# Performance work log

Hardware: AMD Instinct MI355X
Metric: run time of the kernel (lower is better)

## Reference

```python
import jax, jax.numpy as jnp
import numpy as np

B, C, H, W, E, HEADS = 8, 128, 96, 96, 16, 4
HD = C // HEADS

def _ln(x, g, b, eps=1e-5):
    m = jnp.mean(x, axis=-1, keepdims=True)
    v = jnp.mean(jnp.square(x - m), axis=-1, keepdims=True)
    return (x - m) * jax.lax.rsqrt(v + eps) * g + b

def _gelu(x):
    return jax.nn.gelu(x, approximate=False)  # torch nn.GELU default (erf)

def setup_inputs() -> dict:
    key = jax.random.key(0)
    ks = iter(jax.random.split(key, 48))
    def wgt(shape, s=0.02):
        return jax.random.normal(next(ks), shape, jnp.float32) * s
    d = {
        "feature_map": jax.random.normal(next(ks), (B, C, H, W), jnp.float32),
        "hyperedge_scores": jax.random.uniform(next(ks), (B, H * W, E), jnp.float32),
        # norm_node_pre
        "np_g": jnp.ones((C,), jnp.float32), "np_b": jnp.zeros((C,), jnp.float32),
        # MultiheadAttention (self-attn over hyperedges)
        "mha_w_in": wgt((3 * C, C)), "mha_b_in": jnp.zeros((3 * C,), jnp.float32),
        "mha_w_out": wgt((C, C)), "mha_b_out": jnp.zeros((C,), jnp.float32),
        # transformer FFN
        "ffn_w1": wgt((2 * C, C)), "ffn_b1": jnp.zeros((2 * C,), jnp.float32),
        "ffn_w2": wgt((C, 2 * C)), "ffn_b2": jnp.zeros((C,), jnp.float32),
        # shared LayerNorm inside HypergraphTransformerConv (used twice)
        "tnorm_g": jnp.ones((C,), jnp.float32), "tnorm_b": jnp.zeros((C,), jnp.float32),
        # norm_hyper
        "nh_g": jnp.ones((C,), jnp.float32), "nh_b": jnp.zeros((C,), jnp.float32),
        # hyper_proj
        "hp_w": wgt((C, C)), "hp_b": jnp.zeros((C,), jnp.float32),
        # HyperedgeGuidedNodeAttention
        "q_w": wgt((C, C)), "q_b": jnp.zeros((C,), jnp.float32),
        "kv_w": wgt((2 * C, C)), "kv_b": jnp.zeros((2 * C,), jnp.float32),
        # norm_fusion
        "nf_g": jnp.ones((2 * C,), jnp.float32), "nf_b": jnp.zeros((2 * C,), jnp.float32),
        # gate = Linear(2C->C) + LayerNorm(C) + Sigmoid
        "gate_w": wgt((C, 2 * C)), "gate_b": jnp.zeros((C,), jnp.float32),
        "gate_ln_g": jnp.ones((C,), jnp.float32), "gate_ln_b": jnp.zeros((C,), jnp.float32),
        # node_proj
        "nproj_w": wgt((C, C)), "nproj_b": jnp.zeros((C,), jnp.float32),
    }
    return d

def _forward(feature_map, hyperedge_scores, np_g, np_b, mha_w_in, mha_b_in,
             mha_w_out, mha_b_out, ffn_w1, ffn_b1, ffn_w2, ffn_b2,
             tnorm_g, tnorm_b, nh_g, nh_b, hp_w, hp_b, q_w, q_b, kv_w, kv_b,
             nf_g, nf_b, gate_w, gate_b, gate_ln_g, gate_ln_b, nproj_w, nproj_b):
    b, c, h, w = feature_map.shape
    n = h * w
    node = jnp.transpose(feature_map.reshape(b, c, n), (0, 2, 1))   # [B,N,C]
    node = _ln(node, np_g, np_b)
    # hyperedge aggregation: H^T @ X -> [B,E,C]
    hyper = jnp.einsum('bne,bnc->bec', hyperedge_scores, node)
    # --- HypergraphTransformerConv (self-attn over E=16 hyperedges) ---
    qkv = hyper @ mha_w_in.T + mha_b_in                               # [B,E,3C]
    q, k, v = jnp.split(qkv, 3, axis=-1)
    def heads(x):  # [B,E,C] -> [B,h,E,hd]
        return jnp.transpose(x.reshape(b, E, HEADS, HD), (0, 2, 1, 3))
    q, k, v = heads(q), heads(k), heads(v)
    attn = jax.nn.softmax(jnp.einsum('bhqd,bhkd->bhqk', q, k) / np.sqrt(HD), axis=-1)
    ao = jnp.einsum('bhqk,bhkd->bhqd', attn, v)
    ao = jnp.transpose(ao, (0, 2, 1, 3)).reshape(b, E, c)
    ao = ao @ mha_w_out.T + mha_b_out
    x = _ln(hyper + ao, tnorm_g, tnorm_b)
    ffn = _gelu(x @ ffn_w1.T + ffn_b1) @ ffn_w2.T + ffn_b2
    hyper = _ln(x + ffn, tnorm_g, tnorm_b)
    # ---
    hyper = _ln(hyper, nh_g, nh_b)
    hyper = _gelu(hyper @ hp_w.T + hp_b)                              # [B,E,C]
    intra = jnp.einsum('bne,bec->bnc', hyperedge_scores, hyper)       # [B,N,C]
    # HyperedgeGuidedNodeAttention (scale = C**-0.5)
    Q = node @ q_w.T + q_b
    K, V = jnp.split(hyper @ kv_w.T + kv_b, 2, axis=-1)
    a = jax.nn.softmax(jnp.einsum('bnc,bec->bne', Q, K) * (c ** -0.5), axis=-1)
    cross = jnp.einsum('bne,bec->bnc', a, V)
    combined = _ln(jnp.concatenate([intra, cross], axis=-1), nf_g, nf_b)
    gate = jax.nn.sigmoid(_ln(combined @ gate_w.T + gate_b, gate_ln_g, gate_ln_b))
    fused = gate * intra + (1.0 - gate) * cross
    upd = node + fused                                                # dropout in eval mode
    out = _gelu(upd @ nproj_w.T + nproj_b)
    return jnp.transpose(out, (0, 2, 1)).reshape(b, c, h, w)

def reference(feature_map, hyperedge_scores, np_g, np_b, mha_w_in, mha_b_in,
              mha_w_out, mha_b_out, ffn_w1, ffn_b1, ffn_w2, ffn_b2,
              tnorm_g, tnorm_b, nh_g, nh_b, hp_w, hp_b, q_w, q_b, kv_w, kv_b,
              nf_g, nf_b, gate_w, gate_b, gate_ln_g, gate_ln_b, nproj_w, nproj_b):
    return _forward(feature_map, hyperedge_scores, np_g, np_b, mha_w_in, mha_b_in,
                    mha_w_out, mha_b_out, ffn_w1, ffn_b1, ffn_w2, ffn_b2,
                    tnorm_g, tnorm_b, nh_g, nh_b, hp_w, hp_b, q_w, q_b, kv_w, kv_b,
                    nf_g, nf_b, gate_w, gate_b, gate_ln_g, gate_ln_b, nproj_w, nproj_b)
```

## Files before the change

### kernel.cpp

```cpp
#include <hip/hip_runtime.h>

typedef unsigned short bf_t;
typedef unsigned int u32;
typedef short short8 __attribute__((ext_vector_type(8)));
typedef float f32x4 __attribute__((ext_vector_type(4)));

#define NB 8
#define CC 128
#define NN 9216
#define EE 16
#define NT 144

__device__ __forceinline__ float b2f(bf_t u){ return __uint_as_float(((u32)u)<<16); }
__device__ __forceinline__ bf_t f2b(float f){
  u32 u = __float_as_uint(f);
  u = (u + 0x7fffu + ((u>>16)&1u)) >> 16;
  return (bf_t)u;
}
__device__ __forceinline__ float gelu_f(float x){ return 0.5f*x*(1.f+erff(x*0.70710678118654752f)); }
__device__ __forceinline__ float red16(float v){
  #pragma unroll
  for (int m=1;m<16;m<<=1) v += __shfl_xor(v, m, 16);
  return v;
}
__device__ __forceinline__ float grs(float var){
  return rsqrtf(fmaxf(var + 1e-5f, 1e-8f));
}
__device__ __forceinline__ short8 ldw8(const float* __restrict__ p){
  float4 a = *(const float4*)p;
  float4 b = *(const float4*)(p+4);
  short8 o;
  o[0]=(short)f2b(a.x); o[1]=(short)f2b(a.y); o[2]=(short)f2b(a.z); o[3]=(short)f2b(a.w);
  o[4]=(short)f2b(b.x); o[5]=(short)f2b(b.y); o[6]=(short)f2b(b.z); o[7]=(short)f2b(b.w);
  return o;
}

template<int MODE>
__global__ __launch_bounds__(256) void k_pre(float* __restrict__ hacc,
    const float* __restrict__ gw, const float* __restrict__ npw,
    bf_t* __restrict__ gwb, bf_t* __restrict__ npwb,
    const float* __restrict__ w_in, const float* __restrict__ w_out,
    const float* __restrict__ w1, const float* __restrict__ w2,
    const float* __restrict__ hpw, const float* __restrict__ kvw,
    const float* __restrict__ qw,
    bf_t* __restrict__ w_in_b, bf_t* __restrict__ w_out_b,
    bf_t* __restrict__ w1_b, bf_t* __restrict__ w2_b,
    bf_t* __restrict__ hpw_b, bf_t* __restrict__ kvw_b,
    bf_t* __restrict__ qwT_b){
  int i = blockIdx.x*256 + threadIdx.x;
  hacc[i] = 0.f;
  if (MODE >= 1){
    gwb[i]       = f2b(gw[i]);
    gwb[i+16384] = f2b(gw[i+16384]);
    npwb[i]      = f2b(npw[i]);
  }
  if (MODE == 2){
    #pragma unroll
    for (int k=0;k<3;k++) w_in_b[i + k*16384] = f2b(w_in[i + k*16384]);
    w_out_b[i]       = f2b(w_out[i]);
    w1_b[i]          = f2b(w1[i]);
    w1_b[i+16384]    = f2b(w1[i+16384]);
    w2_b[i]          = f2b(w2[i]);
    w2_b[i+16384]    = f2b(w2[i+16384]);
    hpw_b[i]         = f2b(hpw[i]);
    kvw_b[i]         = f2b(kvw[i]);
    kvw_b[i+16384]   = f2b(kvw[i+16384]);
    qwT_b[i]         = f2b(qw[(i&127)*128 + (i>>7)]);
  }
}

template<int BFOUT, int ATOM>
__global__ __launch_bounds__(256,4) void k_ln_agg(const float* __restrict__ fm,
                                                  const float* __restrict__ g,
                                                  const float* __restrict__ bb,
                                                  const float* __restrict__ sc,
                                                  float* __restrict__ nln,
                                                  bf_t* __restrict__ nlnb,
                                                  float* __restrict__ hacc,
                                                  float* __restrict__ part){
  int b = blockIdx.y, n0 = blockIdx.x*64, tid = threadIdx.x;
  __shared__ float xs[128*65];
  __shared__ float scs[64][17];
  __shared__ float ps[4][64], pq[4][64], mrs[2][64];
  const float* base = fm + (size_t)b*CC*NN + n0;
  #pragma unroll
  for (int p=0;p<8;p++){
    int idx = tid + p*256;
    int c = idx>>4, n4 = (idx&15)*4;
    float4 v = *(const float4*)(base + (size_t)c*NN + n4);
    xs[c*65 + n4+0] = v.x; xs[c*65 + n4+1] = v.y;
    xs[c*65 + n4+2] = v.z; xs[c*65 + n4+3] = v.w;
  }
  { int n = tid>>2, e4 = (tid&3)*4;
    float4 sv = *(const float4*)(sc + ((size_t)(b*NN + n0 + n))*EE + e4);
    scs[n][e4+0] = sv.x; scs[n][e4+1] = sv.y;
    scs[n][e4+2] = sv.z; scs[n][e4+3] = sv.w;
  }
  __syncthreads();
  { int cg = tid>>6, n = tid&63;
    float s=0.f, q=0.f;
    #pragma unroll
    for (int c=0;c<32;c++){ float v = xs[(cg*32+c)*65 + n]; s+=v; q+=v*v; }
    ps[cg][n]=s; pq[cg][n]=q;
  }
  __syncthreads();
  if (tid < 64){
    float S = ps[0][tid]+ps[1][tid]+ps[2][tid]+ps[3][tid];
    float Q = pq[0][tid]+pq[1][tid]+pq[2][tid]+pq[3][tid];
    float m = S*(1.f/128.f);
    mrs[0][tid] = m; mrs[1][tid] = grs(Q*(1.f/128.f) - m*m);
  }
  __syncthreads();
  #pragma unroll
  for (int p=0;p<8;p++){
    int idx = tid + p*256;
    int c = idx>>4, n4 = (idx&15)*4;
    float gv = g[c], bv = bb[c];
    float v0 = (xs[c*65+n4+0]-mrs[0][n4+0])*mrs[1][n4+0]*gv + bv;
    float v1 = (xs[c*65+n4+1]-mrs[0][n4+1])*mrs[1][n4+1]*gv + bv;
    float v2 = (xs[c*65+n4+2]-mrs[0][n4+2])*mrs[1][n4+2]*gv + bv;
    float v3 = (xs[c*65+n4+3]-mrs[0][n4+3])*mrs[1][n4+3]*gv + bv;
    xs[c*65+n4+0]=v0; xs[c*65+n4+1]=v1; xs[c*65+n4+2]=v2; xs[c*65+n4+3]=v3;
    if (!BFOUT){
      float4 o; o.x=v0; o.y=v1; o.z=v2; o.w=v3;
      *(float4*)(nln + ((size_t)(b*CC + c))*NN + n0 + n4) = o;
    }
  }
  __syncthreads();
  if (BFOUT){
    #pragma unroll
    for (int p=0;p<4;p++){
      int idx = tid + p*256;
      int n = idx>>4, c8 = (idx&15)*8;
      short8 o;
      #pragma unroll
      for (int j=0;j<8;j++) o[j] = (short)f2b(xs[(c8+j)*65 + n]);
      *(short8*)(nlnb + ((size_t)(b*NN + n0 + n))*CC + c8) = o;
    }
  }
  { int cp = tid&63, eh = tid>>6;
    float a0[4]={0,0,0,0}, a1[4]={0,0,0,0};
    for (int n=0;n<64;n++){
      float x0 = xs[cp*65 + n], x1 = xs[(cp+64)*65 + n];
      #pragma unroll
      for (int j=0;j<4;j++){
        float se = scs[n][eh*4+j];
        a0[j] += se*x0; a1[j] += se*x1;
      }
    }
    if (ATOM){
      #pragma unroll
      for (int j=0;j<4;j++){
        float* hb = hacc + (size_t)(b*EE + eh*4 + j)*CC;
        atomicAdd(hb + cp, a0[j]);
        atomicAdd(hb + cp + 64, a1[j]);
      }
    } else {
      float* pb = part + ((size_t)(b*NT + blockIdx.x)*EE)*CC;
      #pragma unroll
      for (int j=0;j<4;j++){
        pb[(eh*4+j)*CC + cp]      = a0[j];
        pb[(eh*4+j)*CC + cp + 64] = a1[j];
      }
    }
  }
}

__global__ __launch_bounds__(128) void k_red(const float* __restrict__ part,
                                             float* __restrict__ hacc){
  int e = blockIdx.x, b = blockIdx.y, c = threadIdx.x;
  const float* p = part + ((size_t)(b*NT)*EE + e)*CC + c;
  float s0=0.f, s1=0.f, s2=0.f, s3=0.f;
  #pragma unroll
  for (int t=0;t<NT;t+=4){
    s0 += p[(size_t)(t+0)*EE*CC];
    s1 += p[(size_t)(t+1)*EE*CC];
    s2 += p[(size_t)(t+2)*EE*CC];
    s3 += p[(size_t)(t+3)*EE*CC];
  }
  hacc[((size_t)b*EE + e)*CC + c] = (s0+s1)+(s2+s3);
}

template<int K, int NOUT, int ACT, int WB, int NW>
__device__ __forceinline__ void gemm16(const bf_t* A, int SA,
                                       const float* __restrict__ W,
                                       const bf_t* __restrict__ Wb,
                                       const float* __restrict__ bias,
                                       bf_t* O, int SO, int tid){
  int lane = tid&63, wid = tid>>6;
  int m16 = lane&15, quad = lane>>4;
  #pragma unroll
  for (int u=0; u<NOUT/(16*NW); u++){
    int n0 = u*(16*NW) + wid*16;
    f32x4 acc = {0.f,0.f,0.f,0.f};
    #pragma unroll
    for (int k0=0;k0<K;k0+=32){
      short8 af = *(const short8*)(A + m16*SA + k0 + quad*8);
      short8 bfv = WB ? *(const short8*)(Wb + (size_t)(n0+m16)*K + k0 + quad*8)
                      : ldw8(W + (size_t)(n0+m16)*K + k0 + quad*8);
      acc = __builtin_amdgcn_mfma_f32_16x16x32_bf16(af, bfv, acc, 0, 0, 0);
    }
    int col = n0 + m16;
    float bv = bias[col];
    #pragma unroll
    for (int r=0;r<4;r++){
      float v = acc[r] + bv;
      if (ACT) v = gelu_f(v);
      O[(quad*4+r)*SO + col] = f2b(v);
    }
  }
}

#define SP1 136
#define SP2 264
#define SP3 392

template<int WB>
__global__ __launch_bounds__(512) void k_edge(const float* __restrict__ hacc,
    const float* w_in, const float* b_in, const float* w_out, const float* b_out,
    const float* w1, const float* b1, const float* w2, const float* b2v,
    const float* tg, const float* tb, const float* nhg, const float* nhb,
    const float* hpw, const float* hpb, const float* kvw, const float* kvbias,
    const float* qw, const float* qb,
    const bf_t* __restrict__ w_in_b, const bf_t* __restrict__ w_out_b,
    const bf_t* __restrict__ w1_b, const bf_t* __restrict__ w2_b,
    const bf_t* __restrict__ hpw_b, const bf_t* __restrict__ kvw_b,
    const bf_t* __restrict__ qwT_b,
    bf_t* __restrict__ hfw, bf_t* __restrict__ vws,
    bf_t* __restrict__ Ktgb, float* __restrict__ qbK){
  __shared__ __align__(16) bf_t hyp0[16*SP1];
  __shared__ __align__(16) bf_t qkvb[16*SP3];
  __shared__ __align__(16) bf_t aob [16*SP1];
  __shared__ __align__(16) bf_t xnb [16*SP1];
  __shared__ __align__(16) bf_t h1b [16*SP2];
  __shared__ __align__(16) bf_t t2b [16*SP1];
  __shared__ __align__(16) bf_t hfb [16*SP1];
  __shared__ __align__(16) bf_t kvo [16*SP2];
  int b = blockIdx.x, tid = threadIdx.x;
  int lane = tid&63, wid = tid>>6, m16 = lane&15, quad = lane>>4;

  #pragma unroll
  for (int p=0;p<4;p++){
    int idx = tid + p*512;
    int e = idx>>7, c = idx&127;
    hyp0[e*SP1 + c] = f2b(hacc[(size_t)(b*EE + e)*CC + c]);
  }
  __syncthreads();
  gemm16<128,384,0,WB,8>(hyp0, SP1, w_in, w_in_b, b_in, qkvb, SP3, tid);
  __syncthreads();
  if (tid < 256){
    int part = tid&3, hq = tid>>2;
    int h = hq>>4, qi = hq&15;
    int dbase = h*32 + part*8;
    float qv[8];
    #pragma unroll
    for (int j=0;j<8;j++) qv[j] = b2f(qkvb[qi*SP3 + dbase + j]);
    float dot[16];
    #pragma unroll
    for (int kk=0;kk<16;kk++){
      float s = 0.f;
      #pragma unroll
      for (int j=0;j<8;j++) s += qv[j]*b2f(qkvb[kk*SP3 + 128 + dbase + j]);
      dot[kk] = s;
    }
    #pragma unroll
    for (int m=1;m<4;m<<=1){
      #pragma unroll
      for (int kk=0;kk<16;kk++) dot[kk] += __shfl_xor(dot[kk], m, 4);
    }
    const float sc1 = 0.17677669529663687f;
    float mx = -1e30f;
    #pragma unroll
    for (int kk=0;kk<16;kk++){ dot[kk] *= sc1; mx = fmaxf(mx, dot[kk]); }
    float sum = 0.f;
    #pragma unroll
    for (int kk=0;kk<16;kk++){ dot[kk] = __expf(dot[kk]-mx); sum += dot[kk]; }
    float inv = 1.f/sum;
    float ao[8] = {0,0,0,0,0,0,0,0};
    #pragma unroll
    for (int kk=0;kk<16;kk++){
      float p = dot[kk]*inv;
      #pragma unroll
      for (int j=0;j<8;j++) ao[j] += p*b2f(qkvb[kk*SP3 + 256 + dbase + j]);
    }
    #pragma unroll
    for (int j=0;j<8;j++) aob[qi*SP1 + dbase + j] = f2b(ao[j]);
  }
  __syncthreads();
  gemm16<128,128,0,WB,8>(aob, SP1, w_out, w_out_b, b_out, xnb, SP1, tid);
  __syncthreads();
  if (tid < 256){
    int e = tid>>4, i = tid&15;
    float v[8]; float s=0.f, q=0.f;
    #pragma unroll
    for (int j=0;j<8;j++){
      int c = i*8+j;
      v[j] = b2f(hyp0[e*SP1+c]) + b2f(xnb[e*SP1+c]);
      s += v[j]; q += v[j]*v[j];
    }
    s = red16(s); q = red16(q);
    float m = s*(1.f/128.f);
    float rs = grs(q*(1.f/128.f) - m*m);
    #pragma unroll
    for (int j=0;j<8;j++){
      int c = i*8+j;
      xnb[e*SP1+c] = f2b((v[j]-m)*rs*tg[c] + tb[c]);
    }
  }
  __syncthreads();
  gemm16<128,256,1,WB,8>(xnb, SP1, w1, w1_b, b1, h1b, SP2, tid);
  __syncthreads();
  gemm16<256,128,0,WB,8>(h1b, SP2, w2, w2_b, b2v, aob, SP1, tid);
  __syncthreads();
  if (tid < 256){
    int e = tid>>4, i = tid&15;
    float v[8]; float s=0.f, q=0.f;
    #pragma unroll
    for (int j=0;j<8;j++){
      int c = i*8+j;
      v[j] = b2f(xnb[e*SP1+c]) + b2f(aob[e*SP1+c]);
      s += v[j]; q += v[j]*v[j];
    }
    s = red16(s); q = red16(q);
    float m = s*(1.f/128.f);
    float rs = grs(q*(1.f/128.f) - m*m);
    float s2=0.f, q2=0.f;
    #pragma unroll
    for (int j=0;j<8;j++){
      int c = i*8+j;
      v[j] = (v[j]-m)*rs*tg[c] + tb[c];
      s2 += v[j]; q2 += v[j]*v[j];
    }
    s2 = red16(s2); q2 = red16(q2);
    float m2 = s2*(1.f/128.f);
    float rs2 = grs(q2*(1.f/128.f) - m2*m2);
    #pragma unroll
    for (int j=0;j<8;j++){
      int c = i*8+j;
      t2b[e*SP1+c] = f2b((v[j]-m2)*rs2*nhg[c] + nhb[c]);
    }
  }
  __syncthreads();
  gemm16<128,128,1,WB,8>(t2b, SP1, hpw, hpw_b, hpb, hfb, SP1, tid);
  __syncthreads();
  gemm16<128,256,0,WB,8>(hfb, SP1, kvw, kvw_b, kvbias, kvo, SP2, tid);
  __syncthreads();
  #pragma unroll
  for (int p=0;p<4;p++){
    int idx = tid + p*512;
    int e = idx>>7, c = idx&127;
    size_t o = (size_t)(b*EE + e)*CC + c;
    hfw[o] = hfb[e*SP1 + c];
    vws[o] = kvo[e*SP2 + 128 + c];
  }
  {
    int n0 = wid*16;
    f32x4 acc = {0.f,0.f,0.f,0.f};
    #pragma unroll
    for (int k0=0;k0<128;k0+=32){
      short8 a = *(const short8*)(kvo + m16*SP2 + k0 + quad*8);
      short8 bq;
      if (WB){
        bq = *(const short8*)(qwT_b + (size_t)(n0+m16)*128 + k0 + quad*8);
      } else {
        #pragma unroll
        for (int j=0;j<8;j++)
          bq[j] = (short)f2b(qw[(size_t)(k0+quad*8+j)*128 + n0+m16]);
      }
      acc = __builtin_amdgcn_mfma_f32_16x16x32_bf16(a, bq, acc, 0, 0, 0);
    }
    #pragma unroll
    for (int r=0;r<4;r++)
      Ktgb[(size_t)(b*EE + quad*4 + r)*CC + n0 + m16] = f2b(acc[r]);
  }
  if (tid < 256){
    int e = tid>>4, i = tid&15;
    float s = 0.f;
    #pragma unroll
    for (int j=0;j<8;j++) s += qb[i*8+j]*b2f(kvo[e*SP2 + i*8+j]);
    s = red16(s);
    if (i == 0) qbK[b*EE + e] = s;
  }
}

template<int MODE>
__global__ __launch_bounds__(256,3) void k_meganode(
    float* __restrict__ io, const bf_t* __restrict__ nlnb,
    const float* __restrict__ sc,
    const bf_t* __restrict__ hf, const bf_t* __restrict__ vw,
    const bf_t* __restrict__ ktg, const float* __restrict__ qbK,
    const float* __restrict__ nfg, const float* __restrict__ nfb,
    const float* __restrict__ gw, const bf_t* __restrict__ gwb,
    const float* __restrict__ gb,
    const float* __restrict__ glng, const float* __restrict__ glnb,
    const float* __restrict__ npw, const bf_t* __restrict__ npwb,
    const float* __restrict__ npb){
  int tid = threadIdx.x, lane = tid&63, wid = tid>>6;
  int m16 = lane&15, quad = lane>>4;
  int b = blockIdx.y, n0 = blockIdx.x*64;
  __shared__ __align__(16) char sm[34816];
  bf_t* xt  = (bf_t*)(sm);
  bf_t* ktT = (bf_t*)(sm + 17408);
  bf_t* hfT = (bf_t*)(sm + 21760);
  bf_t* vfT = (bf_t*)(sm + 25856);
  bf_t* ash = (bf_t*)(sm + 29952);
  bf_t* ct  = (bf_t*)(sm + 17408);
  float* ot = (float*)(sm);
  const short8 z8 = {0,0,0,0,0,0,0,0};

  if (MODE == 2){
    const bf_t* nb = nlnb + ((size_t)(b*NN + n0))*CC;
    #pragma unroll
    for (int p=0;p<4;p++){
      int idx = tid + p*256;
      int n = idx>>4, c8 = (idx&15)*8;
      *(short8*)&xt[n*136 + c8] = *(const short8*)(nb + (size_t)n*CC + c8);
    }
  } else {
    #pragma unroll
    for (int p=0;p<8;p++){
      int idx = tid + p*256;
      int c = idx>>4, n4 = (idx&15)*4;
      float4 v = *(const float4*)(io + ((size_t)(b*CC + c))*NN + n0 + n4);
      xt[(n4+0)*136 + c] = f2b(v.x);
      xt[(n4+1)*136 + c] = f2b(v.y);
      xt[(n4+2)*136 + c] = f2b(v.z);
      xt[(n4+3)*136 + c] = f2b(v.w);
    }
  }
  { const u32* kp = (const u32*)(ktg + (size_t)b*EE*CC);
    #pragma unroll
    for (int p=0;p<4;p++){
      int idx = tid + p*256;
      int e = idx>>6, c2 = (idx&63)*2;
      *(u32*)&ktT[e*136 + c2] = kp[idx];
    }
  }
  { const u32* hs = (const u32*)(hf + (size_t)b*EE*CC);
    const u32* vs = (const u32*)(vw + (size_t)b*EE*CC);
    #pragma unroll
    for (int p=0;p<4;p++){
      int idx = tid + p*256;
      int e = idx>>6, c2 = (idx&63)*2;
      u32 hv = hs[idx], vv = vs[idx];
      hfT[(c2+0)*16 + e] = (bf_t)(hv&0xffffu);
      hfT[(c2+1)*16 + e] = (bf_t)(hv>>16);
      vfT[(c2+0)*16 + e] = (bf_t)(vv&0xffffu);
      vfT[(c2+1)*16 + e] = (bf_t)(vv>>16);
    }
  }
  __syncthreads();

  f32x4 dacc = {0.f,0.f,0.f,0.f};
  #pragma unroll
  for (int kk=0;kk<4;kk++){
    short8 a = *(const short8*)(xt + (wid*16+m16)*136 + kk*32 + quad*8);
    short8 bfr = *(const short8*)(ktT + m16*136 + kk*32 + quad*8);
    dacc = __builtin_amdgcn_mfma_f32_16x16x32_bf16(a, bfr, dacc, 0, 0, 0);
  }
  { float qbe = qbK[b*EE + m16];
    #pragma unroll
    for (int r=0;r<4;r++){
      float v = (dacc[r] + qbe) * 0.08838834764831845f;
      float m = v;
      #pragma unroll
      for (int msk=1;msk<16;msk<<=1) m = fmaxf(m, __shfl_xor(m, msk, 16));
      float ex = __expf(v - m);
      float s = ex;
      #pragma unroll
      for (int msk=1;msk<16;msk<<=1) s += __shfl_xor(s, msk, 16);
      ash[(wid*16 + quad*4 + r)*16 + m16] = f2b(ex / s);
    }
  }

  short8 scf = z8, asf = z8;
  if (quad < 2){
    const float* sp = sc + ((size_t)(b*NN + n0 + wid*16 + m16))*EE + quad*8;
    float4 u0 = *(const float4*)sp;
    float4 u1 = *(const float4*)(sp+4);
    scf[0]=(short)f2b(u0.x); scf[1]=(short)f2b(u0.y); scf[2]=(short)f2b(u0.z); scf[3]=(short)f2b(u0.w);
    scf[4]=(short)f2b(u1.x); scf[5]=(short)f2b(u1.y); scf[6]=(short)f2b(u1.z); scf[7]=(short)f2b(u1.w);
    asf = *(const short8*)(ash + (wid*16+m16)*16 + quad*8);
  }
  f32x4 acc_it[8], acc_cr[8];
  #pragma unroll
  for (int t=0;t<8;t++){
    short8 bh = z8, bv = z8;
    if (quad < 2){
      bh = *(const short8*)(hfT + (t*16+m16)*16 + quad*8);
      bv = *(const short8*)(vfT + (t*16+m16)*16 + quad*8);
    }
    f32x4 zf = {0.f,0.f,0.f,0.f};
    acc_it[t] = __builtin_amdgcn_mfma_f32_16x16x32_bf16(scf, bh, zf, 0, 0, 0);
    acc_cr[t] = __builtin_amdgcn_mfma_f32_16x16x32_bf16(asf, bv, zf, 0, 0, 0);
  }

  float mean4[4], rstd4[4];
  { float s4[4]={0,0,0,0}, q4[4]={0,0,0,0};
    #pragma unroll
    for (int t=0;t<8;t++)
      #pragma unroll
      for (int r=0;r<4;r++){
        float a = acc_it[t][r], c = acc_cr[t][r];
        s4[r] += a + c; q4[r] += a*a + c*c;
      }
    #pragma unroll
    for (int r=0;r<4;r++){
      s4[r] = red16(s4[r]); q4[r] = red16(q4[r]);
      mean4[r] = s4[r]*(1.f/256.f);
      rstd4[r] = grs(q4[r]*(1.f/256.f) - mean4[r]*mean4[r]);
    }
  }
  __syncthreads();
  short8 af[8];
  #pragma unroll
  for (int r=0;r<4;r++){
    int node = wid*16 + quad*4 + r;
    #pragma unroll
    for (int t=0;t<8;t++){
      int ch = t*16 + m16;
      ct[node*136 + ch] = f2b((acc_it[t][r]-mean4[r])*rstd4[r]*nfg[ch] + nfb[ch]);
    }
  }
  #pragma unroll
  for (int kk=0;kk<4;kk++)
    af[kk] = *(const short8*)(ct + (wid*16+m16)*136 + kk*32 + quad*8);
  #pragma unroll
  for (int r=0;r<4;r++){
    int node = wid*16 + quad*4 + r;
    #pragma unroll
    for (int t=0;t<8;t++){
      int ch = t*16 + m16;
      ct[node*136 + ch] = f2b((acc_cr[t][r]-mean4[r])*rstd4[r]*nfg[128+ch] + nfb[128+ch]);
    }
  }
  #pragma unroll
  for (int kk=0;kk<4;kk++)
    af[4+kk] = *(const short8*)(ct + (wid*16+m16)*136 + kk*32 + quad*8);

  f32x4 acc_g[8];
  #pragma unroll
  for (int t=0;t<8;t++){
    f32x4 a = {0.f,0.f,0.f,0.f};
    #pragma unroll
    for (int kk=0;kk<8;kk++){
      short8 w8 = (MODE >= 1) ? *(const short8*)(gwb + (size_t)(t*16+m16)*256 + kk*32 + quad*8)
                              : ldw8(gw + (size_t)(t*16+m16)*256 + kk*32 + quad*8);
      a = __builtin_amdgcn_mfma_f32_16x16x32_bf16(af[kk], w8, a, 0, 0, 0);
    }
    acc_g[t] = a;
  }

  { float s2[4]={0,0,0,0}, q2[4]={0,0,0,0};
    #pragma unroll
    for (int t=0;t<8;t++){
      float bv = gb[t*16+m16];
      #pragma unroll
      for (int r=0;r<4;r++){
        float v = acc_g[t][r] + bv;
        acc_g[t][r] = v; s2[r] += v; q2[r] += v*v;
      }
    }
    #pragma unroll
    for (int r=0;r<4;r++){ s2[r] = red16(s2[r]); q2[r] = red16(q2[r]); }
    #pragma unroll
    for (int t=0;t<8;t++){
      int col = t*16 + m16;
      float lg = glng[col], lb = glnb[col];
      #pragma unroll
      for (int r=0;r<4;r++){
        float m2 = s2[r]*(1.f/128.f);
        float rs2 = grs(q2[r]*(1.f/128.f) - m2*m2);
        float z = (acc_g[t][r]-m2)*rs2*lg + lb;
        float gs = 1.f/(1.f + __expf(-z));
        int node = wid*16 + quad*4 + r;
        float nld = b2f(xt[node*136 + col]);
        xt[node*136 + col] = f2b(nld + gs*acc_it[t][r] + (1.f-gs)*acc_cr[t][r]);
      }
    }
  }

  short8 bfu[4];
  #pragma unroll
  for (int kk=0;kk<4;kk++)
    bfu[kk] = *(const short8*)(xt + (wid*16+m16)*136 + kk*32 + quad*8);
  __syncthreads();
  #pragma unroll
  for (int mt=0;mt<8;mt++){
    f32x4 o = {0.f,0.f,0.f,0.f};
    #pragma unroll
    for (int kk=0;kk<4;kk++){
      short8 aw = (MODE >= 1) ? *(const short8*)(npwb + (size_t)(mt*16+m16)*128 + kk*32 + quad*8)
                              : ldw8(npw + (size_t)(mt*16+m16)*128 + kk*32 + quad*8);
      o = __builtin_amdgcn_mfma_f32_16x16x32_bf16(aw, bfu[kk], o, 0, 0, 0);
    }
    #pragma unroll
    for (int r=0;r<4;r++){
      int cp = mt*16 + quad*4 + r;
      ot[cp*68 + wid*16 + m16] = gelu_f(o[r] + npb[cp]);
    }
  }
  __syncthreads();
  #pragma unroll
  for (int p=0;p<8;p++){
    int idx = tid + p*256;
    int c = idx>>4, n4 = (idx&15)*4;
    float4 v = *(const float4*)&ot[c*68 + n4];
    *(float4*)(io + ((size_t)(b*CC + c))*NN + n0 + n4) = v;
  }
}

extern "C" void kernel_launch(void* const* d_in, const int* in_sizes, int n_in,
                              void* d_out, int out_size, void* d_ws, size_t ws_size,
                              hipStream_t stream){
  (void)in_sizes; (void)n_in; (void)out_size;
  const float* fm   = (const float*)d_in[0];
  const float* sc   = (const float*)d_in[1];
  const float* npg  = (const float*)d_in[2];
  const float* npb_ = (const float*)d_in[3];
  const float* w_in = (const float*)d_in[4];
  const float* b_in = (const float*)d_in[5];
  const float* w_out= (const float*)d_in[6];
  const float* b_out= (const float*)d_in[7];
  const float* w1   = (const float*)d_in[8];
  const float* b1   = (const float*)d_in[9];
  const float* w2   = (const float*)d_in[10];
  const float* b2v  = (const float*)d_in[11];
  const float* tg   = (const float*)d_in[12];
  const float* tb   = (const float*)d_in[13];
  const float* nhg  = (const float*)d_in[14];
  const float* nhb  = (const float*)d_in[15];
  const float* hpw  = (const float*)d_in[16];
  const float* hpb  = (const float*)d_in[17];
  const float* qw   = (const float*)d_in[18];
  const float* qb   = (const float*)d_in[19];
  const float* kvw  = (const float*)d_in[20];
  const float* kvb  = (const float*)d_in[21];
  const float* nfg  = (const float*)d_in[22];
  const float* nfb  = (const float*)d_in[23];
  const float* gw   = (const float*)d_in[24];
  const float* gb   = (const float*)d_in[25];
  const float* glng = (const float*)d_in[26];
  const float* glnb = (const float*)d_in[27];
  const float* npw  = (const float*)d_in[28];
  const float* npb2 = (const float*)d_in[29];

  float* nln = (float*)d_out;

  char* w = (char*)d_ws;
  float* hacc    = (float*)(w);
  float* qbK     = (float*)(w + 65536);
  bf_t*  hfw     = (bf_t*) (w + 66048);
  bf_t*  vws     = (bf_t*) (w + 98816);
  bf_t*  Ktgb    = (bf_t*) (w + 131584);
  bf_t*  gwb     = (bf_t*) (w + 164352);
  bf_t*  npwb    = (bf_t*) (w + 229888);
  bf_t*  w_in_b  = (bf_t*) (w + 262656);
  bf_t*  w_out_b = (bf_t*) (w + 360960);
  bf_t*  w1_b    = (bf_t*) (w + 393728);
  bf_t*  w2_b    = (bf_t*) (w + 459264);
  bf_t*  hpw_b   = (bf_t*) (w + 524800);
  bf_t*  kvw_b   = (bf_t*) (w + 557568);
  bf_t*  qwT_b   = (bf_t*) (w + 623104);
  bf_t*  nlnb    = (bf_t*) (w + 655872);
  float* part    = (float*)(w + 19530240);
  bool full2 = (ws_size >= (size_t)28967424);
  bool full  = (ws_size >= (size_t)19530240);
  bool pre   = (ws_size >= (size_t)262656);

  if (full2){
    k_pre<2><<<dim3(64), dim3(256), 0, stream>>>(hacc, gw, npw, gwb, npwb,
        w_in, w_out, w1, w2, hpw, kvw, qw,
        w_in_b, w_out_b, w1_b, w2_b, hpw_b, kvw_b, qwT_b);
    k_ln_agg<1,0><<<dim3(NT,8), dim3(256), 0, stream>>>(fm, npg, npb_, sc, nln, nlnb, hacc, part);
    k_red<<<dim3(EE,8), dim3(128), 0, stream>>>(part, hacc);
    k_edge<1><<<dim3(8), dim3(512), 0, stream>>>(hacc, w_in,b_in,w_out,b_out,
        w1,b1,w2,b2v, tg,tb, nhg,nhb, hpw,hpb, kvw,kvb, qw,qb,
        w_in_b, w_out_b, w1_b, w2_b, hpw_b, kvw_b, qwT_b,
        hfw, vws, Ktgb, qbK);
    k_meganode<2><<<dim3(NT,8), dim3(256), 0, stream>>>(nln, nlnb, sc, hfw, vws, Ktgb, qbK,
        nfg, nfb, gw, gwb, gb, glng, glnb, npw, npwb, npb2);
  } else if (full){
    k_pre<2><<<dim3(64), dim3(256), 0, stream>>>(hacc, gw, npw, gwb, npwb,
        w_in, w_out, w1, w2, hpw, kvw, qw,
        w_in_b, w_out_b, w1_b, w2_b, hpw_b, kvw_b, qwT_b);
    k_ln_agg<1,1><<<dim3(NT,8), dim3(256), 0, stream>>>(fm, npg, npb_, sc, nln, nlnb, hacc, part);
    k_edge<1><<<dim3(8), dim3(512), 0, stream>>>(hacc, w_in,b_in,w_out,b_out,
        w1,b1,w2,b2v, tg,tb, nhg,nhb, hpw,hpb, kvw,kvb, qw,qb,
        w_in_b, w_out_b, w1_b, w2_b, hpw_b, kvw_b, qwT_b,
        hfw, vws, Ktgb, qbK);
    k_meganode<2><<<dim3(NT,8), dim3(256), 0, stream>>>(nln, nlnb, sc, hfw, vws, Ktgb, qbK,
        nfg, nfb, gw, gwb, gb, glng, glnb, npw, npwb, npb2);
  } else if (pre){
    k_pre<1><<<dim3(64), dim3(256), 0, stream>>>(hacc, gw, npw, gwb, npwb,
        w_in, w_out, w1, w2, hpw, kvw, qw,
        w_in_b, w_out_b, w1_b, w2_b, hpw_b, kvw_b, qwT_b);
    k_ln_agg<0,1><<<dim3(NT,8), dim3(256), 0, stream>>>(fm, npg, npb_, sc, nln, nlnb, hacc, part);
    k_edge<0><<<dim3(8), dim3(512), 0, stream>>>(hacc, w_in,b_in,w_out,b_out,
        w1,b1,w2,b2v, tg,tb, nhg,nhb, hpw,hpb, kvw,kvb, qw,qb,
        w_in_b, w_out_b, w1_b, w2_b, hpw_b, kvw_b, qwT_b,
        hfw, vws, Ktgb, qbK);
    k_meganode<1><<<dim3(NT,8), dim3(256), 0, stream>>>(nln, nlnb, sc, hfw, vws, Ktgb, qbK,
        nfg, nfb, gw, gwb, gb, glng, glnb, npw, npwb, npb2);
  } else {
    k_pre<0><<<dim3(64), dim3(256), 0, stream>>>(hacc, gw, npw, gwb, npwb,
        w_in, w_out, w1, w2, hpw, kvw, qw,
        w_in_b, w_out_b, w1_b, w2_b, hpw_b, kvw_b, qwT_b);
    k_ln_agg<0,1><<<dim3(NT,8), dim3(256), 0, stream>>>(fm, npg, npb_, sc, nln, nlnb, hacc, part);
    k_edge<0><<<dim3(8), dim3(512), 0, stream>>>(hacc, w_in,b_in,w_out,b_out,
        w1,b1,w2,b2v, tg,tb, nhg,nhb, hpw,hpb, kvw,kvb, qw,qb,
        w_in_b, w_out_b, w1_b, w2_b, hpw_b, kvw_b, qwT_b,
        hfw, vws, Ktgb, qbK);
    k_meganode<0><<<dim3(NT,8), dim3(256), 0, stream>>>(nln, nlnb, sc, hfw, vws, Ktgb, qbK,
        nfg, nfb, gw, gwb, gb, glng, glnb, npw, npwb, npb2);
  }
}
```

Measured before the change: 267.5 us.

## Drop partial-sum reduction kernel, shrink meganode LDS and store output directly

Removes the partial-buffer plus separate reduction kernel path, so hyperedge aggregation always uses global atomics into hacc. In the node kernel, the fused-LayerNorm staging tile is narrowed to 72-wide halves, which cuts shared memory from 34816 to 32000 bytes. The LDS-transposed float4 output store is replaced with direct per-lane global writes, which drops two barriers. The intent is fewer launches and more occupancy, at the cost of atomic contention and less coalesced output stores (each store covers 16 contiguous floats per channel row).

```diff
diff --git a/kernel.cpp b/kernel.cpp
--- a/kernel.cpp
+++ b/kernel.cpp
@@ -69,15 +69,14 @@
   }
 }
 
-template<int BFOUT, int ATOM>
+template<int BFOUT>
 __global__ __launch_bounds__(256,4) void k_ln_agg(const float* __restrict__ fm,
                                                   const float* __restrict__ g,
                                                   const float* __restrict__ bb,
                                                   const float* __restrict__ sc,
                                                   float* __restrict__ nln,
                                                   bf_t* __restrict__ nlnb,
-                                                  float* __restrict__ hacc,
-                                                  float* __restrict__ part){
+                                                  float* __restrict__ hacc){
   int b = blockIdx.y, n0 = blockIdx.x*64, tid = threadIdx.x;
   __shared__ float xs[128*65];
   __shared__ float scs[64][17];
@@ -148,37 +147,13 @@
         a0[j] += se*x0; a1[j] += se*x1;
       }
     }
-    if (ATOM){
-      #pragma unroll
-      for (int j=0;j<4;j++){
-        float* hb = hacc + (size_t)(b*EE + eh*4 + j)*CC;
-        atomicAdd(hb + cp, a0[j]);
-        atomicAdd(hb + cp + 64, a1[j]);
-      }
-    } else {
-      float* pb = part + ((size_t)(b*NT + blockIdx.x)*EE)*CC;
-      #pragma unroll
-      for (int j=0;j<4;j++){
-        pb[(eh*4+j)*CC + cp]      = a0[j];
-        pb[(eh*4+j)*CC + cp + 64] = a1[j];
-      }
-    }
-  }
-}
-
-__global__ __launch_bounds__(128) void k_red(const float* __restrict__ part,
-                                             float* __restrict__ hacc){
-  int e = blockIdx.x, b = blockIdx.y, c = threadIdx.x;
-  const float* p = part + ((size_t)(b*NT)*EE + e)*CC + c;
-  float s0=0.f, s1=0.f, s2=0.f, s3=0.f;
-  #pragma unroll
-  for (int t=0;t<NT;t+=4){
-    s0 += p[(size_t)(t+0)*EE*CC];
-    s1 += p[(size_t)(t+1)*EE*CC];
-    s2 += p[(size_t)(t+2)*EE*CC];
-    s3 += p[(size_t)(t+3)*EE*CC];
-  }
-  hacc[((size_t)b*EE + e)*CC + c] = (s0+s1)+(s2+s3);
+    #pragma unroll
+    for (int j=0;j<4;j++){
+      float* hb = hacc + (size_t)(b*EE + eh*4 + j)*CC;
+      atomicAdd(hb + cp, a0[j]);
+      atomicAdd(hb + cp + 64, a1[j]);
+    }
+  }
 }
 
 template<int K, int NOUT, int ACT, int WB, int NW>
@@ -398,14 +373,13 @@
   int tid = threadIdx.x, lane = tid&63, wid = tid>>6;
   int m16 = lane&15, quad = lane>>4;
   int b = blockIdx.y, n0 = blockIdx.x*64;
-  __shared__ __align__(16) char sm[34816];
+  __shared__ __align__(16) char sm[32000];
   bf_t* xt  = (bf_t*)(sm);
   bf_t* ktT = (bf_t*)(sm + 17408);
   bf_t* hfT = (bf_t*)(sm + 21760);
   bf_t* vfT = (bf_t*)(sm + 25856);
   bf_t* ash = (bf_t*)(sm + 29952);
   bf_t* ct  = (bf_t*)(sm + 17408);
-  float* ot = (float*)(sm);
   const short8 z8 = {0,0,0,0,0,0,0,0};
 
   if (MODE == 2){
@@ -514,29 +488,35 @@
   __syncthreads();
   short8 af[8];
   #pragma unroll
-  for (int r=0;r<4;r++){
-    int node = wid*16 + quad*4 + r;
-    #pragma unroll
-    for (int t=0;t<8;t++){
-      int ch = t*16 + m16;
-      ct[node*136 + ch] = f2b((acc_it[t][r]-mean4[r])*rstd4[r]*nfg[ch] + nfb[ch]);
-    }
-  }
-  #pragma unroll
-  for (int kk=0;kk<4;kk++)
-    af[kk] = *(const short8*)(ct + (wid*16+m16)*136 + kk*32 + quad*8);
-  #pragma unroll
-  for (int r=0;r<4;r++){
-    int node = wid*16 + quad*4 + r;
-    #pragma unroll
-    for (int t=0;t<8;t++){
-      int ch = t*16 + m16;
-      ct[node*136 + ch] = f2b((acc_cr[t][r]-mean4[r])*rstd4[r]*nfg[128+ch] + nfb[128+ch]);
-    }
-  }
-  #pragma unroll
-  for (int kk=0;kk<4;kk++)
-    af[4+kk] = *(const short8*)(ct + (wid*16+m16)*136 + kk*32 + quad*8);
+  for (int s=0;s<2;s++){
+    #pragma unroll
+    for (int r=0;r<4;r++){
+      int node = wid*16 + quad*4 + r;
+      #pragma unroll
+      for (int t=0;t<4;t++){
+        int ch = (s*4+t)*16 + m16;
+        ct[node*72 + t*16 + m16] = f2b((acc_it[s*4+t][r]-mean4[r])*rstd4[r]*nfg[ch] + nfb[ch]);
+      }
+    }
+    #pragma unroll
+    for (int k2=0;k2<2;k2++)
+      af[s*2+k2] = *(const short8*)(ct + (wid*16+m16)*72 + k2*32 + quad*8);
+  }
+  #pragma unroll
+  for (int s=0;s<2;s++){
+    #pragma unroll
+    for (int r=0;r<4;r++){
+      int node = wid*16 + quad*4 + r;
+      #pragma unroll
+      for (int t=0;t<4;t++){
+        int ch = (s*4+t)*16 + m16;
+        ct[node*72 + t*16 + m16] = f2b((acc_cr[s*4+t][r]-mean4[r])*rstd4[r]*nfg[128+ch] + nfb[128+ch]);
+      }
+    }
+    #pragma unroll
+    for (int k2=0;k2<2;k2++)
+      af[4+s*2+k2] = *(const short8*)(ct + (wid*16+m16)*72 + k2*32 + quad*8);
+  }
 
   f32x4 acc_g[8];
   #pragma unroll
@@ -584,7 +564,6 @@
   #pragma unroll
   for (int kk=0;kk<4;kk++)
     bfu[kk] = *(const short8*)(xt + (wid*16+m16)*136 + kk*32 + quad*8);
-  __syncthreads();
   #pragma unroll
   for (int mt=0;mt<8;mt++){
     f32x4 o = {0.f,0.f,0.f,0.f};
@@ -597,16 +576,8 @@
     #pragma unroll
     for (int r=0;r<4;r++){
       int cp = mt*16 + quad*4 + r;
-      ot[cp*68 + wid*16 + m16] = gelu_f(o[r] + npb[cp]);
-    }
-  }
-  __syncthreads();
-  #pragma unroll
-  for (int p=0;p<8;p++){
-    int idx = tid + p*256;
-    int c = idx>>4, n4 = (idx&15)*4;
-    float4 v = *(const float4*)&ot[c*68 + n4];
-    *(float4*)(io + ((size_t)(b*CC + c))*NN + n0 + n4) = v;
+      io[((size_t)(b*CC + cp))*NN + n0 + wid*16 + m16] = gelu_f(o[r] + npb[cp]);
+    }
   }
 }
 
@@ -663,28 +634,14 @@
   bf_t*  kvw_b   = (bf_t*) (w + 557568);
   bf_t*  qwT_b   = (bf_t*) (w + 623104);
   bf_t*  nlnb    = (bf_t*) (w + 655872);
-  float* part    = (float*)(w + 19530240);
-  bool full2 = (ws_size >= (size_t)28967424);
   bool full  = (ws_size >= (size_t)19530240);
   bool pre   = (ws_size >= (size_t)262656);
 
-  if (full2){
+  if (full){
     k_pre<2><<<dim3(64), dim3(256), 0, stream>>>(hacc, gw, npw, gwb, npwb,
         w_in, w_out, w1, w2, hpw, kvw, qw,
         w_in_b, w_out_b, w1_b, w2_b, hpw_b, kvw_b, qwT_b);
-    k_ln_agg<1,0><<<dim3(NT,8), dim3(256), 0, stream>>>(fm, npg, npb_, sc, nln, nlnb, hacc, part);
-    k_red<<<dim3(EE,8), dim3(128), 0, stream>>>(part, hacc);
-    k_edge<1><<<dim3(8), dim3(512), 0, stream>>>(hacc, w_in,b_in,w_out,b_out,
-        w1,b1,w2,b2v, tg,tb, nhg,nhb, hpw,hpb, kvw,kvb, qw,qb,
-        w_in_b, w_out_b, w1_b, w2_b, hpw_b, kvw_b, qwT_b,
-        hfw, vws, Ktgb, qbK);
-    k_meganode<2><<<dim3(NT,8), dim3(256), 0, stream>>>(nln, nlnb, sc, hfw, vws, Ktgb, qbK,
-        nfg, nfb, gw, gwb, gb, glng, glnb, npw, npwb, npb2);
-  } else if (full){
-    k_pre<2><<<dim3(64), dim3(256), 0, stream>>>(hacc, gw, npw, gwb, npwb,
-        w_in, w_out, w1, w2, hpw, kvw, qw,
-        w_in_b, w_out_b, w1_b, w2_b, hpw_b, kvw_b, qwT_b);
-    k_ln_agg<1,1><<<dim3(NT,8), dim3(256), 0, stream>>>(fm, npg, npb_, sc, nln, nlnb, hacc, part);
+    k_ln_agg<1><<<dim3(NT,8), dim3(256), 0, stream>>>(fm, npg, npb_, sc, nln, nlnb, hacc);
     k_edge<1><<<dim3(8), dim3(512), 0, stream>>>(hacc, w_in,b_in,w_out,b_out,
         w1,b1,w2,b2v, tg,tb, nhg,nhb, hpw,hpb, kvw,kvb, qw,qb,
         w_in_b, w_out_b, w1_b, w2_b, hpw_b, kvw_b, qwT_b,
@@ -695,7 +652,7 @@
     k_pre<1><<<dim3(64), dim3(256), 0, stream>>>(hacc, gw, npw, gwb, npwb,
         w_in, w_out, w1, w2, hpw, kvw, qw,
         w_in_b, w_out_b, w1_b, w2_b, hpw_b, kvw_b, qwT_b);
-    k_ln_agg<0,1><<<dim3(NT,8), dim3(256), 0, stream>>>(fm, npg, npb_, sc, nln, nlnb, hacc, part);
+    k_ln_agg<0><<<dim3(NT,8), dim3(256), 0, stream>>>(fm, npg, npb_, sc, nln, nlnb, hacc);
     k_edge<0><<<dim3(8), dim3(512), 0, stream>>>(hacc, w_in,b_in,w_out,b_out,
         w1,b1,w2,b2v, tg,tb, nhg,nhb, hpw,hpb, kvw,kvb, qw,qb,
         w_in_b, w_out_b, w1_b, w2_b, hpw_b, kvw_b, qwT_b,
@@ -706,7 +663,7 @@
     k_pre<0><<<dim3(64), dim3(256), 0, stream>>>(hacc, gw, npw, gwb, npwb,
         w_in, w_out, w1, w2, hpw, kvw, qw,
         w_in_b, w_out_b, w1_b, w2_b, hpw_b, kvw_b, qwT_b);
-    k_ln_agg<0,1><<<dim3(NT,8), dim3(256), 0, stream>>>(fm, npg, npb_, sc, nln, nlnb, hacc, part);
+    k_ln_agg<0><<<dim3(NT,8), dim3(256), 0, stream>>>(fm, npg, npb_, sc, nln, nlnb, hacc);
     k_edge<0><<<dim3(8), dim3(512), 0, stream>>>(hacc, w_in,b_in,w_out,b_out,
         w1,b1,w2,b2v, tg,tb, nhg,nhb, hpw,hpb, kvw,kvb, qw,qb,
         w_in_b, w_out_b, w1_b, w2_b, hpw_b, kvw_b, qwT_b,
```

Measured after the change: 261.1 us. 1.02x faster.
